# Optimization experiments

Measured on AMD Instinct MI355X. Metric: run time of the kernel, lower is better.

Reference implementation:

```python
import jax, jax.numpy as jnp
import numpy as np

N = 100000          # nodes
E = 1000000         # edges (before self loops)
F_IN = 128          # node feature dim
HEADS = [4, 2, 2]   # gat_heads
D = 48              # per-head out channels (hardcoded in module)
G = 64              # number of graphs in batch
FC_DIM = 192
OUT_DIM = 96
NEG_SLOPE = 0.2     # PyG GATConv default


def setup_inputs() -> dict:
    key = jax.random.key(0)
    ks = jax.random.split(key, 32)
    d = {
        "x": jax.random.normal(ks[0], (N, F_IN), jnp.float32),
        "edge_index": jax.random.randint(ks[1], (2, E), 0, N, dtype=jnp.int64),
        "batch": jnp.sort(jax.random.randint(ks[2], (N,), 0, G, dtype=jnp.int64)),
    }
    in_ch = F_IN
    k = 3
    for i, h in enumerate(HEADS):
        d[f"W{i}"] = jax.random.normal(ks[k], (in_ch, h * D), jnp.float32) / np.sqrt(in_ch); k += 1
        d[f"att_src{i}"] = jax.random.normal(ks[k], (h, D), jnp.float32) * 0.1; k += 1
        d[f"att_dst{i}"] = jax.random.normal(ks[k], (h, D), jnp.float32) * 0.1; k += 1
        d[f"bias{i}"] = jnp.zeros((h * D,), jnp.float32)
        in_ch = h * D
    d["fcW1"] = jax.random.normal(ks[k], (in_ch, FC_DIM), jnp.float32) / np.sqrt(in_ch); k += 1
    d["fcb1"] = jnp.zeros((FC_DIM,), jnp.float32)
    d["fcW2"] = jax.random.normal(ks[k], (FC_DIM, OUT_DIM), jnp.float32) / np.sqrt(FC_DIM); k += 1
    d["fcb2"] = jnp.zeros((OUT_DIM,), jnp.float32)
    return d


def _gat_layer(x, W, att_src, att_dst, bias, src, dst, heads):
    n = x.shape[0]
    h = (x @ W).reshape(n, heads, D)                    # [N,H,D]
    a_src = jnp.sum(h * att_src, axis=-1)               # [N,H]
    a_dst = jnp.sum(h * att_dst, axis=-1)               # [N,H]
    e = jax.nn.leaky_relu(a_src[src] + a_dst[dst], NEG_SLOPE)   # [Et,H]
    # segment softmax over incoming edges at each destination node
    m = jax.ops.segment_max(e, dst, num_segments=n)
    e = jnp.exp(e - m[dst])
    denom = jax.ops.segment_sum(e, dst, num_segments=n)
    alpha = e / (denom[dst] + 1e-16)                    # [Et,H]
    msg = h[src] * alpha[..., None]                     # [Et,H,D]
    out = jax.ops.segment_sum(msg, dst, num_segments=n) # [N,H,D]
    return out.reshape(n, heads * D) + bias


def reference(x, edge_index, batch,
              W0, att_src0, att_dst0, bias0,
              W1, att_src1, att_dst1, bias1,
              W2, att_src2, att_dst2, bias2,
              fcW1, fcb1, fcW2, fcb2):
    n = x.shape[0]
    loops = jnp.arange(n, dtype=edge_index.dtype)
    src = jnp.concatenate([edge_index[0], loops])   # add self loops (PyG default)
    dst = jnp.concatenate([edge_index[1], loops])
    x = jax.nn.relu(_gat_layer(x, W0, att_src0, att_dst0, bias0, src, dst, HEADS[0]))
    x = jax.nn.relu(_gat_layer(x, W1, att_src1, att_dst1, bias1, src, dst, HEADS[1]))
    x = jax.nn.relu(_gat_layer(x, W2, att_src2, att_dst2, bias2, src, dst, HEADS[2]))
    # global mean pool over graphs
    sums = jax.ops.segment_sum(x, batch, num_segments=G)
    counts = jax.ops.segment_sum(jnp.ones((n, 1), x.dtype), batch, num_segments=G)
    pooled = sums / jnp.maximum(counts, 1.0)
    h = jax.nn.relu(pooled @ fcW1 + fcb1)
    return h @ fcW2 + fcb2
```

## Files before the change

### kernel.cpp

```cpp
#include <hip/hip_runtime.h>

#define CAP 48
#define DD 48
#define BSH 8
#define NBUCK_MAX 400
#define CHUNK_MAX 4300

typedef short v8s __attribute__((ext_vector_type(8)));
typedef float v4f __attribute__((ext_vector_type(4)));
typedef float v2f __attribute__((ext_vector_type(2)));

__device__ __forceinline__ unsigned int bf16r(float f) {
    unsigned int u = __float_as_uint(f);
    return (u + 0x7FFFu + ((u >> 16) & 1u)) >> 16;
}

__device__ __forceinline__ v8s ld_frag(const ushort* p) {
    const uint2* q = reinterpret_cast<const uint2*>(p);
    uint2 a = q[0], b = q[1];
    union { unsigned int u[4]; v8s v; } t;
    t.u[0] = a.x; t.u[1] = a.y; t.u[2] = b.x; t.u[3] = b.y;
    return t.v;
}


__global__ void hist_kernel(const int* __restrict__ ei, int E, int N, int nbuck,
                            int* __restrict__ Hh) {
    __shared__ int lhist[NBUCK_MAX];
    int blk = blockIdx.x, t = threadIdx.x;
    int Et = E + N;
    int chunk = (Et + 255) >> 8;
    int lo = blk * chunk, hi = min(Et, lo + chunk);
    for (int i = t; i < nbuck; i += 256) lhist[i] = 0;
    __syncthreads();
    for (int e = lo + t; e < hi; e += 256) {
        int d = (e < E) ? ei[E + e] : (e - E);
        atomicAdd(&lhist[d >> BSH], 1);
    }
    __syncthreads();
    for (int b = t; b < nbuck; b += 256) Hh[b * 256 + blk] = lhist[b];
}

__global__ void scan_bucket_kernel(int* __restrict__ Hh, int* __restrict__ btot) {
    int b = blockIdx.x, lane = threadIdx.x;
    uint4 v = reinterpret_cast<uint4*>(Hh)[b * 64 + lane];
    unsigned s0 = v.x, s1 = s0 + v.y, s2 = s1 + v.z, s3 = s2 + v.w;
    unsigned incl = s3;
#pragma unroll
    for (int off = 1; off < 64; off <<= 1) {
        unsigned tmp = __shfl_up(incl, off);
        if (lane >= off) incl += tmp;
    }
    unsigned excl = incl - s3;
    reinterpret_cast<uint4*>(Hh)[b * 64 + lane] =
        make_uint4(excl, excl + s0, excl + s1, excl + s2);
    if (lane == 63) btot[b] = (int)incl;
}

__global__ void scan_base_kernel(const int* __restrict__ btot, int* __restrict__ bbase, int nbuck) {
    int lane = threadIdx.x;
    int carry = 0;
    int nch = (nbuck + 63) >> 6;
    for (int c = 0; c < nch; c++) {
        int idx = c * 64 + lane;
        int val = (idx < nbuck) ? btot[idx] : 0;
        int incl = val;
#pragma unroll
        for (int off = 1; off < 64; off <<= 1) {
            int tmp = __shfl_up(incl, off);
            if (lane >= off) incl += tmp;
        }
        if (idx < nbuck) bbase[idx] = carry + incl - val;
        carry += __shfl(incl, 63);
    }
    if (lane == 0) bbase[nbuck] = carry;
}

__global__ void add_base_kernel(int* __restrict__ Hh, const int* __restrict__ bbase) {
    Hh[blockIdx.x * 256 + threadIdx.x] += bbase[blockIdx.x];
}

__global__ void scatter_kernel(const int* __restrict__ ei, int E, int N, int nbuck,
                               const int* __restrict__ Hh, unsigned int* __restrict__ P) {
    __shared__ unsigned int sp[CHUNK_MAX];
    __shared__ int ga[CHUNK_MAX];
    __shared__ int lhist[NBUCK_MAX], lbaseL[NBUCK_MAX], lbaseG[NBUCK_MAX], lcur[NBUCK_MAX];
    int blk = blockIdx.x, t = threadIdx.x;
    int Et = E + N;
    int chunk = (Et + 255) >> 8;
    int lo = blk * chunk, hi = min(Et, lo + chunk);
    for (int i = t; i < nbuck; i += 256) { lhist[i] = 0; lcur[i] = 0; }
    __syncthreads();
    for (int e = lo + t; e < hi; e += 256) {
        int d = (e < E) ? ei[E + e] : (e - E);
        atomicAdd(&lhist[d >> BSH], 1);
    }
    __syncthreads();
    if (t < 64) {
        int lane = t, carry = 0;
        int nch = (nbuck + 63) >> 6;
        for (int c = 0; c < nch; c++) {
            int idx = c * 64 + lane;
            int val = (idx < nbuck) ? lhist[idx] : 0;
            int incl = val;
#pragma unroll
            for (int off = 1; off < 64; off <<= 1) {
                int tmp = __shfl_up(incl, off);
                if (lane >= off) incl += tmp;
            }
            if (idx < nbuck) {
                lbaseL[idx] = carry + incl - val;
                lbaseG[idx] = Hh[idx * 256 + blk];
            }
            carry += __shfl(incl, 63);
        }
    }
    __syncthreads();
    for (int e = lo + t; e < hi; e += 256) {
        int s, d;
        if (e < E) { s = ei[e]; d = ei[E + e]; } else { s = e - E; d = e - E; }
        int b = d >> BSH;
        int lpos = atomicAdd(&lcur[b], 1);
        int loc = lbaseL[b] + lpos;
        sp[loc] = ((unsigned)(d & 255) << 24) | (unsigned)s;
        ga[loc] = lbaseG[b] + lpos;
    }
    __syncthreads();
    int len = hi - lo;
    for (int i = t; i < len; i += 256) P[ga[i]] = sp[i];
}

__global__ void buildadj_kernel(const unsigned int* __restrict__ P, const int* __restrict__ bbase,
                                int* __restrict__ adj, int* __restrict__ cro, int N) {
    __shared__ int slab[256 * CAP];
    __shared__ int cntL[256];
    __shared__ int wsum[4];
    int b = blockIdx.x, t = threadIdx.x;
    int n0 = b << BSH;
    int nodes = min(256, N - n0);
    cntL[t] = 0;
    __syncthreads();
    int lo = bbase[b], hi = bbase[b + 1];
    for (int i = lo + t; i < hi; i += 256) {
        unsigned p = P[i];
        int dloc = (int)(p >> 24);
        int s = (int)(p & 0x1FFFFu);
        int lpos = atomicAdd(&cntL[dloc], 1);
        if (lpos < CAP) slab[dloc * CAP + lpos] = s;
    }
    __syncthreads();
    int capped = min(cntL[t], CAP);
    int lane = t & 63, wv = t >> 6;
    int incl = capped;
#pragma unroll
    for (int off = 1; off < 64; off <<= 1) {
        int tmp = __shfl_up(incl, off);
        if (lane >= off) incl += tmp;
    }
    if (lane == 63) wsum[wv] = incl;
    __syncthreads();
    int wbase = 0;
    if (wv > 0) wbase += wsum[0];
    if (wv > 1) wbase += wsum[1];
    if (wv > 2) wbase += wsum[2];
    int startL = wbase + incl - capped;
    if (t < nodes) {
        int start = n0 * CAP + startL;
        cro[n0 + t] = start | (capped << 25);
        for (int j = 0; j < capped; j++) adj[start + j] = slab[t * CAP + j];
    }
}

__global__ void cast_x_kernel(const float* __restrict__ x, unsigned int* __restrict__ xb, long n2) {
    long i = (long)blockIdx.x * blockDim.x + threadIdx.x;
    if (i >= n2) return;
    float2 v = reinterpret_cast<const float2*>(x)[i];
    xb[i] = bf16r(v.x) | (bf16r(v.y) << 16);
}

__global__ void convw_kernel(const float* __restrict__ W, ushort* __restrict__ WT, int K, int NC) {
    int i = blockIdx.x * blockDim.x + threadIdx.x;
    if (i >= K * NC) return;
    int k = i / NC, n = i % NC;
    WT[n * K + k] = (ushort)bf16r(W[i]);
}

__global__ void attw_kernel(const float* __restrict__ W, const float* __restrict__ as_,
                            const float* __restrict__ ad_, ushort* __restrict__ WT,
                            int K, int NC, int H2) {
    int tid = blockIdx.x * blockDim.x + threadIdx.x;
    if (tid >= K * H2) return;
    int k = tid / H2, idx = tid % H2;
    int h = idx >> 1;
    const float* att = (idx & 1) ? ad_ : as_;
    float s = 0.f;
    for (int d = 0; d < 48; d++) s += W[k * NC + h * 48 + d] * att[h * 48 + d];
    WT[(long)(NC + idx) * K + k] = (ushort)bf16r(s);
}

template<int K, int NCT, int HEADS, int NBY>
__global__ void gemm_mfma(const ushort* __restrict__ Xb, const ushort* __restrict__ WT,
                          ushort* __restrict__ Hb, float* __restrict__ asrc,
                          float* __restrict__ adst, int N) {
    __shared__ ushort XT_l[128 * 40];
    __shared__ ushort WT_l[112 * 40];
    int tid = threadIdx.x;
    int wv = tid >> 6, lane = tid & 63;
    int m = lane & 15, quad = lane >> 4;
    int bid = blockIdx.x;
    int ybl = (NBY == 2) ? (bid & 1) : 0;
    int xbl = (NBY == 2) ? (bid >> 1) : bid;
    int rb = xbl * 128;
    int c0 = ybl * 96;
    int h0 = 2 * ybl;
    int mw = wv * 32;
    v4f acc[2][7];
#pragma unroll
    for (int mi = 0; mi < 2; mi++)
#pragma unroll
        for (int nb = 0; nb < 7; nb++) acc[mi][nb] = (v4f){0.f, 0.f, 0.f, 0.f};

    for (int k0 = 0; k0 < K; k0 += 32) {
#pragma unroll
        for (int t = 0; t < 2; t++) {
            int ch = tid + t * 256;
            int r = ch >> 2, kq = ch & 3;
            int rg = rb + r;
            uint4 v = make_uint4(0u, 0u, 0u, 0u);
            if (rg < N) v = *reinterpret_cast<const uint4*>(&Xb[(long)rg * K + k0 + kq * 8]);
            uint2* d = reinterpret_cast<uint2*>(&XT_l[r * 40 + kq * 8]);
            d[0] = make_uint2(v.x, v.y);
            d[1] = make_uint2(v.z, v.w);
        }
#pragma unroll
        for (int t = 0; t < 2; t++) {
            int ch = tid + t * 256;
            if (ch < 448) {
                int wr = ch >> 2, kq = ch & 3;
                uint4 v = make_uint4(0u, 0u, 0u, 0u);
                if (wr < 96)
                    v = *reinterpret_cast<const uint4*>(&WT[(long)(c0 + wr) * K + k0 + kq * 8]);
                else if (wr < 100)
                    v = *reinterpret_cast<const uint4*>(&WT[(long)(NCT + 4 * ybl + (wr - 96)) * K + k0 + kq * 8]);
                uint2* d = reinterpret_cast<uint2*>(&WT_l[wr * 40 + kq * 8]);
                d[0] = make_uint2(v.x, v.y);
                d[1] = make_uint2(v.z, v.w);
            }
        }
        __syncthreads();
        v8s af[2], bf[7];
        af[0] = ld_frag(&XT_l[(mw + m) * 40 + quad * 8]);
        af[1] = ld_frag(&XT_l[(mw + 16 + m) * 40 + quad * 8]);
#pragma unroll
        for (int nb = 0; nb < 7; nb++)
            bf[nb] = ld_frag(&WT_l[(nb * 16 + m) * 40 + quad * 8]);
#pragma unroll
        for (int mi = 0; mi < 2; mi++)
#pragma unroll
            for (int nb = 0; nb < 7; nb++)
                acc[mi][nb] = __builtin_amdgcn_mfma_f32_16x16x32_bf16(af[mi], bf[nb], acc[mi][nb], 0, 0, 0);
        __syncthreads();
    }

#pragma unroll
    for (int mi = 0; mi < 2; mi++)
#pragma unroll
        for (int r = 0; r < 4; r++) {
            int R = rb + mw + mi * 16 + quad * 4 + r;
            if (R < N) {
#pragma unroll
                for (int nb = 0; nb < 6; nb++)
                    Hb[(long)R * NCT + c0 + nb * 16 + m] = (ushort)bf16r(acc[mi][nb][r]);
            }
        }

#pragma unroll
    for (int mi = 0; mi < 2; mi++)
#pragma unroll
        for (int r = 0; r < 4; r++) {
            int R = rb + mw + mi * 16 + quad * 4 + r;
            if (m < 4 && R < N) {
                float v = acc[mi][6][r];
                int h = h0 + (m >> 1);
                if (m & 1) adst[R * HEADS + h] = v;
                else       asrc[R * HEADS + h] = v;
            }
        }
}

template<int OUT, int HEADS, int EPW, bool OBF16>
__global__ void agg_kernel(const unsigned int* __restrict__ Hb,
                           const float* __restrict__ asrc, const float* __restrict__ adst,
                           const int* __restrict__ adj, const int* __restrict__ cro,
                           const float* __restrict__ bias,
                           unsigned int* __restrict__ Ob, float* __restrict__ Of, int N) {
    constexpr int LPE = 64 / EPW;
    constexpr int ROWU = OUT / 2;
    static_assert(LPE * 6 == ROWU, "lane chunk is 6 uints");
    __shared__ float wlds[4][HEADS][65];
    __shared__ int   slds[4][64];
    int wv = threadIdx.x >> 6;
    int lane = threadIdx.x & 63;
    int esub = lane / LPE;
    int lp   = lane % LPE;
    int n = blockIdx.x * 4 + wv;
    bool valid = (n < N);
    int nn = valid ? n : 0;
    unsigned craw = (unsigned)cro[nn];
    int deg = (int)(craw >> 25);
    int start = (int)(craw & 0x1FFFFFFu);
    int s = 0;
    if (lane < deg) s = adj[start + lane];
    slds[wv][lane] = s;
    __builtin_amdgcn_wave_barrier();

    int c = lp * 12;
    int head = c / DD;

    uint3 A0, A1, B0, B1;
    B0 = make_uint3(0u, 0u, 0u); B1 = B0;
    {
        int s0 = slds[wv][esub];
        const unsigned int* p0 = &Hb[(long)s0 * ROWU + lp * 6];
        A0 = *reinterpret_cast<const uint3*>(p0);
        A1 = *reinterpret_cast<const uint3*>(p0 + 3);
        if (EPW < deg) {
            int s1 = slds[wv][EPW + esub];
            const unsigned int* p1 = &Hb[(long)s1 * ROWU + lp * 6];
            B0 = *reinterpret_cast<const uint3*>(p1);
            B1 = *reinterpret_cast<const uint3*>(p1 + 3);
        }
    }

    float av[HEADS], dvv[HEADS];
    if constexpr (HEADS == 4) {
        float4 t = *reinterpret_cast<const float4*>(&asrc[s * 4]);
        av[0] = t.x; av[1] = t.y; av[2] = t.z; av[3] = t.w;
        float4 u = *reinterpret_cast<const float4*>(&adst[nn * 4]);
        dvv[0] = u.x; dvv[1] = u.y; dvv[2] = u.z; dvv[3] = u.w;
    } else {
        float2 t = *reinterpret_cast<const float2*>(&asrc[s * 2]);
        av[0] = t.x; av[1] = t.y;
        float2 u = *reinterpret_cast<const float2*>(&adst[nn * 2]);
        dvv[0] = u.x; dvv[1] = u.y;
    }
    float w[HEADS], den[HEADS];
#pragma unroll
    for (int h = 0; h < HEADS; h++) {
        float e = av[h] + dvv[h];
        e = (e < 0.f) ? 0.2f * e : e;
        w[h] = (lane < deg) ? __expf(e) : 0.f;
        wlds[wv][h][lane] = w[h];
    }
#pragma unroll
    for (int h = 0; h < HEADS; h++) {
        float dsum = w[h];
#pragma unroll
        for (int off = 1; off < 64; off <<= 1) dsum += __shfl_xor(dsum, off);
        den[h] = dsum;
    }
    __builtin_amdgcn_wave_barrier();

    const float* wrow = &wlds[wv][head][0];
    v2f a0 = (v2f){0.f, 0.f}, a1 = (v2f){0.f, 0.f}, a2 = (v2f){0.f, 0.f};
    v2f a3 = (v2f){0.f, 0.f}, a4 = (v2f){0.f, 0.f}, a5 = (v2f){0.f, 0.f};

    auto ACC6 = [&](const uint3& lo, const uint3& hi, float wgt) {
        v2f p;
        p.x = __uint_as_float(lo.x << 16); p.y = __uint_as_float(lo.x & 0xFFFF0000u); a0 += wgt * p;
        p.x = __uint_as_float(lo.y << 16); p.y = __uint_as_float(lo.y & 0xFFFF0000u); a1 += wgt * p;
        p.x = __uint_as_float(lo.z << 16); p.y = __uint_as_float(lo.z & 0xFFFF0000u); a2 += wgt * p;
        p.x = __uint_as_float(hi.x << 16); p.y = __uint_as_float(hi.x & 0xFFFF0000u); a3 += wgt * p;
        p.x = __uint_as_float(hi.y << 16); p.y = __uint_as_float(hi.y & 0xFFFF0000u); a4 += wgt * p;
        p.x = __uint_as_float(hi.z << 16); p.y = __uint_as_float(hi.z & 0xFFFF0000u); a5 += wgt * p;
    };

    int nb = (deg + 2 * EPW - 1) / (2 * EPW);
    for (int it = 0; it < nb; it++) {
        int nbase = (it + 1) * 2 * EPW;
        uint3 nA0 = make_uint3(0u, 0u, 0u), nA1 = nA0, nB0 = nA0, nB1 = nA0;
        if (nbase < deg) {
            int s0n = slds[wv][nbase + esub];
            const unsigned int* p0 = &Hb[(long)s0n * ROWU + lp * 6];
            nA0 = *reinterpret_cast<const uint3*>(p0);
            nA1 = *reinterpret_cast<const uint3*>(p0 + 3);
            if (nbase + EPW < deg) {
                int s1n = slds[wv][nbase + EPW + esub];
                const unsigned int* p1 = &Hb[(long)s1n * ROWU + lp * 6];
                nB0 = *reinterpret_cast<const uint3*>(p1);
                nB1 = *reinterpret_cast<const uint3*>(p1 + 3);
            }
        }
        int e0 = it * 2 * EPW + esub;
        float w0 = wrow[e0], w1 = wrow[e0 + EPW];
        ACC6(A0, A1, w0);
        ACC6(B0, B1, w1);
        A0 = nA0; A1 = nA1; B0 = nB0; B1 = nB1;
    }

#pragma unroll
    for (int off = LPE; off < 64; off <<= 1) {
        a0.x += __shfl_xor(a0.x, off); a0.y += __shfl_xor(a0.y, off);
        a1.x += __shfl_xor(a1.x, off); a1.y += __shfl_xor(a1.y, off);
        a2.x += __shfl_xor(a2.x, off); a2.y += __shfl_xor(a2.y, off);
        a3.x += __shfl_xor(a3.x, off); a3.y += __shfl_xor(a3.y, off);
        a4.x += __shfl_xor(a4.x, off); a4.y += __shfl_xor(a4.y, off);
        a5.x += __shfl_xor(a5.x, off); a5.y += __shfl_xor(a5.y, off);
    }

    if (valid && esub == 0) {
        float denh;
        if constexpr (HEADS == 4) {
            denh = (head == 0) ? den[0] : (head == 1) ? den[1] : (head == 2) ? den[2] : den[3];
        } else {
            denh = (head == 0) ? den[0] : den[1];
        }
        float invd = 1.f / (denh + 1e-16f);
        float o[12];
        o[0]  = fmaxf(fmaf(a0.x, invd, bias[c + 0]), 0.f);
        o[1]  = fmaxf(fmaf(a0.y, invd, bias[c + 1]), 0.f);
        o[2]  = fmaxf(fmaf(a1.x, invd, bias[c + 2]), 0.f);
        o[3]  = fmaxf(fmaf(a1.y, invd, bias[c + 3]), 0.f);
        o[4]  = fmaxf(fmaf(a2.x, invd, bias[c + 4]), 0.f);
        o[5]  = fmaxf(fmaf(a2.y, invd, bias[c + 5]), 0.f);
        o[6]  = fmaxf(fmaf(a3.x, invd, bias[c + 6]), 0.f);
        o[7]  = fmaxf(fmaf(a3.y, invd, bias[c + 7]), 0.f);
        o[8]  = fmaxf(fmaf(a4.x, invd, bias[c + 8]), 0.f);
        o[9]  = fmaxf(fmaf(a4.y, invd, bias[c + 9]), 0.f);
        o[10] = fmaxf(fmaf(a5.x, invd, bias[c + 10]), 0.f);
        o[11] = fmaxf(fmaf(a5.y, invd, bias[c + 11]), 0.f);
        if (OBF16) {
            uint3 pk1, pk2;
            pk1.x = bf16r(o[0])  | (bf16r(o[1])  << 16);
            pk1.y = bf16r(o[2])  | (bf16r(o[3])  << 16);
            pk1.z = bf16r(o[4])  | (bf16r(o[5])  << 16);
            pk2.x = bf16r(o[6])  | (bf16r(o[7])  << 16);
            pk2.y = bf16r(o[8])  | (bf16r(o[9])  << 16);
            pk2.z = bf16r(o[10]) | (bf16r(o[11]) << 16);
            unsigned int* dst = &Ob[(long)n * ROWU + lp * 6];
            *reinterpret_cast<uint3*>(dst)     = pk1;
            *reinterpret_cast<uint3*>(dst + 3) = pk2;
        } else {
            float* dst = &Of[(long)n * OUT + c];
            *reinterpret_cast<float4*>(dst)     = make_float4(o[0], o[1], o[2],  o[3]);
            *reinterpret_cast<float4*>(dst + 4) = make_float4(o[4], o[5], o[6],  o[7]);
            *reinterpret_cast<float4*>(dst + 8) = make_float4(o[8], o[9], o[10], o[11]);
        }
    }
}

__global__ void pool_kernel(const unsigned int* __restrict__ Ob, const int* __restrict__ batch,
                            float* __restrict__ sums, float* __restrict__ counts, int N) {
    int grp = threadIdx.x >> 6;
    int lane = threadIdx.x & 63;
    int n0 = (blockIdx.x * 8 + grp) * 64;
    if (n0 >= N) return;
    int nend = min(N, n0 + 64);
    bool act = (lane < 48);
    float ax = 0.f, ay = 0.f; int cl = 0;
    int cur = batch[n0];
    for (int n = n0; n < nend; n++) {
        int g = batch[n];
        unsigned v = act ? Ob[(long)n * 48 + lane] : 0u;
        float vx = __uint_as_float(v << 16);
        float vy = __uint_as_float(v & 0xFFFF0000u);
        if (g != cur) {
            if (act) {
                atomicAdd(&sums[cur * 96 + lane * 2],     ax);
                atomicAdd(&sums[cur * 96 + lane * 2 + 1], ay);
            }
            if (lane == 48) atomicAdd(&counts[cur], (float)cl);
            ax = 0.f; ay = 0.f; cl = 0; cur = g;
        }
        ax += vx; ay += vy; cl++;
    }
    if (act) {
        atomicAdd(&sums[cur * 96 + lane * 2],     ax);
        atomicAdd(&sums[cur * 96 + lane * 2 + 1], ay);
    }
    if (lane == 48) atomicAdd(&counts[cur], (float)cl);
}

__global__ void fc_kernel(const float* __restrict__ sums, const float* __restrict__ counts,
                          const float* __restrict__ W1, const float* __restrict__ b1,
                          const float* __restrict__ W2, const float* __restrict__ b2,
                          float* __restrict__ out) {
    __shared__ float p[96];
    __shared__ float h1[192];
    int g = blockIdx.x, tid = threadIdx.x;
    if (tid < 96) p[tid] = sums[g * 96 + tid] / fmaxf(counts[g], 1.0f);
    __syncthreads();
    float s = b1[tid];
    for (int c = 0; c < 96; c++) s = fmaf(p[c], W1[c * 192 + tid], s);
    h1[tid] = fmaxf(s, 0.f);
    __syncthreads();
    if (tid < 96) {
        float s2 = b2[tid];
        for (int j = 0; j < 192; j++) s2 = fmaf(h1[j], W2[j * 96 + tid], s2);
        out[g * 96 + tid] = s2;
    }
}

extern "C" void kernel_launch(void* const* d_in, const int* in_sizes, int n_in,
                              void* d_out, int out_size, void* d_ws, size_t ws_size,
                              hipStream_t stream) {
    const float* x     = (const float*)d_in[0];
    const int*   ei    = (const int*)d_in[1];
    const int*   batch = (const int*)d_in[2];
    const float* W0  = (const float*)d_in[3];
    const float* as0 = (const float*)d_in[4];
    const float* ad0 = (const float*)d_in[5];
    const float* b0  = (const float*)d_in[6];
    const float* W1  = (const float*)d_in[7];
    const float* as1 = (const float*)d_in[8];
    const float* ad1 = (const float*)d_in[9];
    const float* b1  = (const float*)d_in[10];
    const float* W2  = (const float*)d_in[11];
    const float* as2 = (const float*)d_in[12];
    const float* ad2 = (const float*)d_in[13];
    const float* b2  = (const float*)d_in[14];
    const float* fcW1 = (const float*)d_in[15];
    const float* fcb1 = (const float*)d_in[16];
    const float* fcW2 = (const float*)d_in[17];
    const float* fcb2 = (const float*)d_in[18];

    const int N = in_sizes[0] / 128;
    const int E = in_sizes[1] / 2;
    const int nbuck = (N + 255) >> 8;

    char* ws = (char*)d_ws;
    unsigned int* Xb   = (unsigned int*)ws;
    unsigned int* Hb   = (unsigned int*)(ws + (size_t)N * 256);
    unsigned int* Ob   = (unsigned int*)(ws + (size_t)N * 640);
    float*        ASRC = (float*)(ws + (size_t)N * 1408);
    float*        ADST = (float*)(ws + (size_t)N * 1424);
    int*          ADJ  = (int*)(ws + (size_t)N * 1440);
    int*          CRO  = (int*)(ws + (size_t)N * 1632);
    float*        SUMS = (float*)(ws + (size_t)N * 1636);
    float*        COUNTS = SUMS + 64 * 96;
    ushort*       WT0  = (ushort*)(COUNTS + 64);
    ushort*       WT1  = WT0 + 200 * 128;
    ushort*       WT2  = WT1 + 100 * 192;
    char*         tail = (char*)(WT2 + 100 * 96);
    int*          HIST = (int*)tail;
    int*          BTOT = (int*)(tail + NBUCK_MAX * 256 * 4);
    int*          BBASE = (int*)(tail + NBUCK_MAX * 256 * 4 + NBUCK_MAX * 4);
    unsigned int* P    = (unsigned int*)(tail + NBUCK_MAX * 260 * 4 + 64);

    hipMemsetAsync(SUMS, 0, (64 * 96 + 64) * 4, stream);

    hist_kernel<<<256, 256, 0, stream>>>(ei, E, N, nbuck, HIST);
    scan_bucket_kernel<<<nbuck, 64, 0, stream>>>(HIST, BTOT);
    scan_base_kernel<<<1, 64, 0, stream>>>(BTOT, BBASE, nbuck);
    add_base_kernel<<<nbuck, 256, 0, stream>>>(HIST, BBASE);
    scatter_kernel<<<256, 256, 0, stream>>>(ei, E, N, nbuck, HIST, P);
    buildadj_kernel<<<nbuck, 256, 0, stream>>>(P, BBASE, ADJ, CRO, N);

    long n2 = (long)N * 64;
    cast_x_kernel<<<(int)((n2 + 255) / 256), 256, 0, stream>>>(x, Xb, n2);
    convw_kernel<<<(128 * 192 + 255) / 256, 256, 0, stream>>>(W0, WT0, 128, 192);
    convw_kernel<<<(192 * 96 + 255) / 256, 256, 0, stream>>>(W1, WT1, 192, 96);
    convw_kernel<<<(96 * 96 + 255) / 256, 256, 0, stream>>>(W2, WT2, 96, 96);
    attw_kernel<<<4, 256, 0, stream>>>(W0, as0, ad0, WT0, 128, 192, 8);
    attw_kernel<<<3, 256, 0, stream>>>(W1, as1, ad1, WT1, 192, 96, 4);
    attw_kernel<<<2, 256, 0, stream>>>(W2, as2, ad2, WT2, 96, 96, 4);

    int gb = (N + 127) / 128;

    gemm_mfma<128, 192, 4, 2><<<gb * 2, 256, 0, stream>>>((const ushort*)Xb, WT0,
                                                          (ushort*)Hb, ASRC, ADST, N);
    agg_kernel<192, 4, 4, true><<<(N + 3) / 4, 256, 0, stream>>>(Hb, ASRC, ADST, ADJ, CRO, b0, Ob, nullptr, N);

    gemm_mfma<192, 96, 2, 1><<<gb, 256, 0, stream>>>((const ushort*)Ob, WT1,
                                                     (ushort*)Hb, ASRC, ADST, N);
    agg_kernel<96, 2, 8, true><<<(N + 3) / 4, 256, 0, stream>>>(Hb, ASRC, ADST, ADJ, CRO, b1, Ob, nullptr, N);

    gemm_mfma<96, 96, 2, 1><<<gb, 256, 0, stream>>>((const ushort*)Ob, WT2,
                                                    (ushort*)Hb, ASRC, ADST, N);
    agg_kernel<96, 2, 8, true><<<(N + 3) / 4, 256, 0, stream>>>(Hb, ASRC, ADST, ADJ, CRO, b2, Ob, nullptr, N);

    pool_kernel<<<(N + 511) / 512, 512, 0, stream>>>(Ob, batch, SUMS, COUNTS, N);
    fc_kernel<<<64, 192, 0, stream>>>(SUMS, COUNTS, fcW1, fcb1, fcW2, fcb2, (float*)d_out);
}
```

Baseline: 474.6 us.

## Split layer-0 aggregation into column groups and merge prep/scan kernels

Replaces the layer-0 aggregation kernel with a grouped variant that splits each 192-wide node row into three 64-column groups, each handled by a separate block, using 16-byte loads and 8 edges per pass. Block IDs are interleaved so that blocks for the same node range run close together, which should help L2 reuse of gathered rows. The intent is more parallelism and smaller per-lane register footprint for the widest gather. It also merges the cast and weight-conversion kernels into one prep launch and fuses the bucket base scan with the add, cutting launch overhead. The cost is that the adjacency list and attention weights are re-read and the softmax recomputed three times per node.

```diff
diff --git a/kernel.cpp b/kernel.cpp
--- a/kernel.cpp
+++ b/kernel.cpp
@@ -57,27 +57,32 @@
     if (lane == 63) btot[b] = (int)incl;
 }
 
-__global__ void scan_base_kernel(const int* __restrict__ btot, int* __restrict__ bbase, int nbuck) {
-    int lane = threadIdx.x;
-    int carry = 0;
-    int nch = (nbuck + 63) >> 6;
-    for (int c = 0; c < nch; c++) {
-        int idx = c * 64 + lane;
-        int val = (idx < nbuck) ? btot[idx] : 0;
-        int incl = val;
-#pragma unroll
-        for (int off = 1; off < 64; off <<= 1) {
-            int tmp = __shfl_up(incl, off);
-            if (lane >= off) incl += tmp;
-        }
-        if (idx < nbuck) bbase[idx] = carry + incl - val;
-        carry += __shfl(incl, 63);
-    }
-    if (lane == 0) bbase[nbuck] = carry;
-}
-
-__global__ void add_base_kernel(int* __restrict__ Hh, const int* __restrict__ bbase) {
-    Hh[blockIdx.x * 256 + threadIdx.x] += bbase[blockIdx.x];
+__global__ void base_kernel(int* __restrict__ Hh, const int* __restrict__ btot,
+                            int* __restrict__ bbase, int nbuck) {
+    __shared__ int sbase, stot;
+    int b = blockIdx.x, t = threadIdx.x;
+    if (t < 64) {
+        int carry = 0;
+        int nch = (nbuck + 63) >> 6;
+        for (int c = 0; c < nch; c++) {
+            int idx = c * 64 + t;
+            int val = (idx < nbuck) ? btot[idx] : 0;
+            int incl = val;
+#pragma unroll
+            for (int off = 1; off < 64; off <<= 1) {
+                int tmp = __shfl_up(incl, off);
+                if (t >= off) incl += tmp;
+            }
+            if (idx == b) sbase = carry + incl - val;
+            carry += __shfl(incl, 63);
+        }
+        if (t == 0) stot = carry;
+    }
+    __syncthreads();
+    int base = sbase;
+    Hh[b * 256 + t] += base;
+    if (t == 0) bbase[b] = base;
+    if (b == nbuck - 1 && t == 1) bbase[nbuck] = stot;
 }
 
 __global__ void scatter_kernel(const int* __restrict__ ei, int E, int N, int nbuck,
@@ -171,24 +176,16 @@
     }
 }
 
-__global__ void cast_x_kernel(const float* __restrict__ x, unsigned int* __restrict__ xb, long n2) {
-    long i = (long)blockIdx.x * blockDim.x + threadIdx.x;
-    if (i >= n2) return;
-    float2 v = reinterpret_cast<const float2*>(x)[i];
-    xb[i] = bf16r(v.x) | (bf16r(v.y) << 16);
-}
-
-__global__ void convw_kernel(const float* __restrict__ W, ushort* __restrict__ WT, int K, int NC) {
-    int i = blockIdx.x * blockDim.x + threadIdx.x;
+__device__ __forceinline__ void convw_body(const float* __restrict__ W, ushort* __restrict__ WT,
+                                           int K, int NC, int i) {
     if (i >= K * NC) return;
     int k = i / NC, n = i % NC;
     WT[n * K + k] = (ushort)bf16r(W[i]);
 }
 
-__global__ void attw_kernel(const float* __restrict__ W, const float* __restrict__ as_,
-                            const float* __restrict__ ad_, ushort* __restrict__ WT,
-                            int K, int NC, int H2) {
-    int tid = blockIdx.x * blockDim.x + threadIdx.x;
+__device__ __forceinline__ void attw_body(const float* __restrict__ W, const float* __restrict__ as_,
+                                          const float* __restrict__ ad_, ushort* __restrict__ WT,
+                                          int K, int NC, int H2, int tid) {
     if (tid >= K * H2) return;
     int k = tid / H2, idx = tid % H2;
     int h = idx >> 1;
@@ -196,6 +193,44 @@
     float s = 0.f;
     for (int d = 0; d < 48; d++) s += W[k * NC + h * 48 + d] * att[h * 48 + d];
     WT[(long)(NC + idx) * K + k] = (ushort)bf16r(s);
+}
+
+#define C0B 96
+#define C1B 72
+#define C2B 36
+#define A0B 4
+#define A1B 3
+#define A2B 2
+
+__global__ void prep_kernel(const float* __restrict__ x, unsigned int* __restrict__ xb, long n2,
+                            const float* __restrict__ W0, const float* __restrict__ W1,
+                            const float* __restrict__ W2,
+                            const float* __restrict__ as0, const float* __restrict__ ad0,
+                            const float* __restrict__ as1, const float* __restrict__ ad1,
+                            const float* __restrict__ as2, const float* __restrict__ ad2,
+                            ushort* __restrict__ WT0, ushort* __restrict__ WT1,
+                            ushort* __restrict__ WT2, int nbcast) {
+    int bid = blockIdx.x, t = threadIdx.x;
+    if (bid < nbcast) {
+        long i = (long)bid * 256 + t;
+        if (i < n2) {
+            float2 v = reinterpret_cast<const float2*>(x)[i];
+            xb[i] = bf16r(v.x) | (bf16r(v.y) << 16);
+        }
+        return;
+    }
+    bid -= nbcast;
+    if (bid < C0B)                 { convw_body(W0, WT0, 128, 192, bid * 256 + t); return; }
+    bid -= C0B;
+    if (bid < C1B)                 { convw_body(W1, WT1, 192,  96, bid * 256 + t); return; }
+    bid -= C1B;
+    if (bid < C2B)                 { convw_body(W2, WT2,  96,  96, bid * 256 + t); return; }
+    bid -= C2B;
+    if (bid < A0B)                 { attw_body(W0, as0, ad0, WT0, 128, 192, 8, bid * 256 + t); return; }
+    bid -= A0B;
+    if (bid < A1B)                 { attw_body(W1, as1, ad1, WT1, 192,  96, 4, bid * 256 + t); return; }
+    bid -= A1B;
+    attw_body(W2, as2, ad2, WT2, 96, 96, 4, bid * 256 + t);
 }
 
 template<int K, int NCT, int HEADS, int NBY>
@@ -286,6 +321,125 @@
                 else       asrc[R * HEADS + h] = v;
             }
         }
+}
+
+__global__ void agg_group_kernel(const unsigned int* __restrict__ Hb,
+                                 const float* __restrict__ asrc, const float* __restrict__ adst,
+                                 const int* __restrict__ adj, const int* __restrict__ cro,
+                                 const float* __restrict__ bias,
+                                 unsigned int* __restrict__ Ob, int N, int nq) {
+    __shared__ float wlds[4][2][65];
+    __shared__ int   slds[4][64];
+    int bid = blockIdx.x;
+    int k = bid & 7, r = bid >> 3;
+    int g, i;
+    if (k == 0 || k == 3 || k == 6)      { g = 0; i = r * 3 + (k / 3); }
+    else if (k == 1 || k == 4 || k == 7) { g = 1; i = r * 3 + ((k - 1) / 3); }
+    else                                 { g = 2; i = r * 2 + ((k - 2) / 3); }
+    if (i >= nq) return;
+    int wv = threadIdx.x >> 6, lane = threadIdx.x & 63;
+    int esub = lane >> 3;
+    int lp   = lane & 7;
+    int n = i * 4 + wv;
+    bool valid = (n < N);
+    int nn = valid ? n : 0;
+    unsigned craw = (unsigned)cro[nn];
+    int deg = (int)(craw >> 25);
+    int start = (int)(craw & 0x1FFFFFFu);
+    int s = 0;
+    if (lane < deg) s = adj[start + lane];
+    slds[wv][lane] = s;
+    __builtin_amdgcn_wave_barrier();
+
+    int hA = (g * 64) / 48;
+    int cb = g * 64 + lp * 8;
+    int hl = cb / 48 - hA;
+
+    uint4 A = make_uint4(0u, 0u, 0u, 0u), B = A;
+    {
+        int s0 = slds[wv][esub];
+        A = *reinterpret_cast<const uint4*>(&Hb[(long)s0 * 96 + g * 32 + lp * 4]);
+        if (8 < deg) {
+            int s1 = slds[wv][8 + esub];
+            B = *reinterpret_cast<const uint4*>(&Hb[(long)s1 * 96 + g * 32 + lp * 4]);
+        }
+    }
+
+    float4 t = *reinterpret_cast<const float4*>(&asrc[(long)s * 4]);
+    float4 u = *reinterpret_cast<const float4*>(&adst[(long)nn * 4]);
+    float avA = (hA == 0) ? t.x : (hA == 1) ? t.y : t.z;
+    float avB = (hA == 0) ? t.y : (hA == 1) ? t.z : t.w;
+    float dvA = (hA == 0) ? u.x : (hA == 1) ? u.y : u.z;
+    float dvB = (hA == 0) ? u.y : (hA == 1) ? u.z : u.w;
+    float eA = avA + dvA; eA = (eA < 0.f) ? 0.2f * eA : eA;
+    float eB = avB + dvB; eB = (eB < 0.f) ? 0.2f * eB : eB;
+    float wA = (lane < deg) ? __expf(eA) : 0.f;
+    float wB = (lane < deg) ? __expf(eB) : 0.f;
+    wlds[wv][0][lane] = wA;
+    wlds[wv][1][lane] = wB;
+    float denA = wA, denB = wB;
+#pragma unroll
+    for (int off = 1; off < 64; off <<= 1) {
+        denA += __shfl_xor(denA, off);
+        denB += __shfl_xor(denB, off);
+    }
+    __builtin_amdgcn_wave_barrier();
+
+    v2f a0 = (v2f){0.f, 0.f}, a1 = a0, a2 = a0, a3 = a0;
+    auto ACC8 = [&](const uint4& h, float wgt) {
+        v2f p;
+        p.x = __uint_as_float(h.x << 16); p.y = __uint_as_float(h.x & 0xFFFF0000u); a0 += wgt * p;
+        p.x = __uint_as_float(h.y << 16); p.y = __uint_as_float(h.y & 0xFFFF0000u); a1 += wgt * p;
+        p.x = __uint_as_float(h.z << 16); p.y = __uint_as_float(h.z & 0xFFFF0000u); a2 += wgt * p;
+        p.x = __uint_as_float(h.w << 16); p.y = __uint_as_float(h.w & 0xFFFF0000u); a3 += wgt * p;
+    };
+
+    int nbi = (deg + 15) >> 4;
+    for (int it = 0; it < nbi; it++) {
+        int nbase = (it + 1) * 16;
+        uint4 nA = make_uint4(0u, 0u, 0u, 0u), nB = nA;
+        if (nbase < deg) {
+            int s0n = slds[wv][nbase + esub];
+            nA = *reinterpret_cast<const uint4*>(&Hb[(long)s0n * 96 + g * 32 + lp * 4]);
+            if (nbase + 8 < deg) {
+                int s1n = slds[wv][nbase + 8 + esub];
+                nB = *reinterpret_cast<const uint4*>(&Hb[(long)s1n * 96 + g * 32 + lp * 4]);
+            }
+        }
+        float w0 = wlds[wv][hl][it * 16 + esub];
+        float w1 = wlds[wv][hl][it * 16 + 8 + esub];
+        ACC8(A, w0);
+        ACC8(B, w1);
+        A = nA; B = nB;
+    }
+
+#pragma unroll
+    for (int off = 8; off < 64; off <<= 1) {
+        a0.x += __shfl_xor(a0.x, off); a0.y += __shfl_xor(a0.y, off);
+        a1.x += __shfl_xor(a1.x, off); a1.y += __shfl_xor(a1.y, off);
+        a2.x += __shfl_xor(a2.x, off); a2.y += __shfl_xor(a2.y, off);
+        a3.x += __shfl_xor(a3.x, off); a3.y += __shfl_xor(a3.y, off);
+    }
+
+    if (valid && esub == 0) {
+        float denh = hl ? denB : denA;
+        float invd = 1.f / (denh + 1e-16f);
+        float o[8];
+        o[0] = fmaxf(fmaf(a0.x, invd, bias[cb + 0]), 0.f);
+        o[1] = fmaxf(fmaf(a0.y, invd, bias[cb + 1]), 0.f);
+        o[2] = fmaxf(fmaf(a1.x, invd, bias[cb + 2]), 0.f);
+        o[3] = fmaxf(fmaf(a1.y, invd, bias[cb + 3]), 0.f);
+        o[4] = fmaxf(fmaf(a2.x, invd, bias[cb + 4]), 0.f);
+        o[5] = fmaxf(fmaf(a2.y, invd, bias[cb + 5]), 0.f);
+        o[6] = fmaxf(fmaf(a3.x, invd, bias[cb + 6]), 0.f);
+        o[7] = fmaxf(fmaf(a3.y, invd, bias[cb + 7]), 0.f);
+        uint4 pk;
+        pk.x = bf16r(o[0]) | (bf16r(o[1]) << 16);
+        pk.y = bf16r(o[2]) | (bf16r(o[3]) << 16);
+        pk.z = bf16r(o[4]) | (bf16r(o[5]) << 16);
+        pk.w = bf16r(o[6]) | (bf16r(o[7]) << 16);
+        *reinterpret_cast<uint4*>(&Ob[(long)n * 96 + g * 32 + lp * 4]) = pk;
+    }
 }
 
 template<int OUT, int HEADS, int EPW, bool OBF16>
@@ -362,8 +516,7 @@
     __builtin_amdgcn_wave_barrier();
 
     const float* wrow = &wlds[wv][head][0];
-    v2f a0 = (v2f){0.f, 0.f}, a1 = (v2f){0.f, 0.f}, a2 = (v2f){0.f, 0.f};
-    v2f a3 = (v2f){0.f, 0.f}, a4 = (v2f){0.f, 0.f}, a5 = (v2f){0.f, 0.f};
+    v2f a0 = (v2f){0.f, 0.f}, a1 = a0, a2 = a0, a3 = a0, a4 = a0, a5 = a0;
 
     auto ACC6 = [&](const uint3& lo, const uint3& hi, float wgt) {
         v2f p;
@@ -551,25 +704,23 @@
 
     hist_kernel<<<256, 256, 0, stream>>>(ei, E, N, nbuck, HIST);
     scan_bucket_kernel<<<nbuck, 64, 0, stream>>>(HIST, BTOT);
-    scan_base_kernel<<<1, 64, 0, stream>>>(BTOT, BBASE, nbuck);
-    add_base_kernel<<<nbuck, 256, 0, stream>>>(HIST, BBASE);
+    base_kernel<<<nbuck, 256, 0, stream>>>(HIST, BTOT, BBASE, nbuck);
     scatter_kernel<<<256, 256, 0, stream>>>(ei, E, N, nbuck, HIST, P);
     buildadj_kernel<<<nbuck, 256, 0, stream>>>(P, BBASE, ADJ, CRO, N);
 
     long n2 = (long)N * 64;
-    cast_x_kernel<<<(int)((n2 + 255) / 256), 256, 0, stream>>>(x, Xb, n2);
-    convw_kernel<<<(128 * 192 + 255) / 256, 256, 0, stream>>>(W0, WT0, 128, 192);
-    convw_kernel<<<(192 * 96 + 255) / 256, 256, 0, stream>>>(W1, WT1, 192, 96);
-    convw_kernel<<<(96 * 96 + 255) / 256, 256, 0, stream>>>(W2, WT2, 96, 96);
-    attw_kernel<<<4, 256, 0, stream>>>(W0, as0, ad0, WT0, 128, 192, 8);
-    attw_kernel<<<3, 256, 0, stream>>>(W1, as1, ad1, WT1, 192, 96, 4);
-    attw_kernel<<<2, 256, 0, stream>>>(W2, as2, ad2, WT2, 96, 96, 4);
+    int nbcast = (int)((n2 + 255) / 256);
+    int prep_grid = nbcast + C0B + C1B + C2B + A0B + A1B + A2B;
+    prep_kernel<<<prep_grid, 256, 0, stream>>>(x, Xb, n2, W0, W1, W2,
+                                               as0, ad0, as1, ad1, as2, ad2,
+                                               WT0, WT1, WT2, nbcast);
 
     int gb = (N + 127) / 128;
+    int nq = (N + 3) / 4;
 
     gemm_mfma<128, 192, 4, 2><<<gb * 2, 256, 0, stream>>>((const ushort*)Xb, WT0,
                                                           (ushort*)Hb, ASRC, ADST, N);
-    agg_kernel<192, 4, 4, true><<<(N + 3) / 4, 256, 0, stream>>>(Hb, ASRC, ADST, ADJ, CRO, b0, Ob, nullptr, N);
+    agg_group_kernel<<<8 * ((nq + 1) / 2), 256, 0, stream>>>(Hb, ASRC, ADST, ADJ, CRO, b0, Ob, N, nq);
 
     gemm_mfma<192, 96, 2, 1><<<gb, 256, 0, stream>>>((const ushort*)Ob, WT1,
                                                      (ushort*)Hb, ASRC, ADST, N);
```

After: 569.8 us. 20.1% more time.
